# Kernel tuning notes

Measured on AMD Instinct MI355X. Metric: run time of the kernel, lower is better.

## Reference

```python
import jax, jax.numpy as jnp
import numpy as np

EPS = 1e-5  # torch BatchNorm default eps
B, C, T, NOUT, NCLS = 4096, 32, 512, 16, 4


def setup_inputs() -> dict:
    key = jax.random.key(0)
    ks = jax.random.split(key, 12)
    s = lambda k, shape: jax.random.normal(k, shape, jnp.float32) * 0.05
    return {
        "de": jax.random.normal(ks[0], (B, C, T), jnp.float32),
        "adj": jax.random.normal(ks[1], (B, C, C), jnp.float32),  # unused by forward (module recomputes corr)
        "dw_w": s(ks[2], (C, 1, 3)),      # depthwise Conv1d weight [C,1,3]
        "dw_b": s(ks[3], (C,)),
        "pw_w": s(ks[4], (C, C)),          # pointwise 1x1 conv [out,in]
        "pw_b": s(ks[5], (C,)),
        "bn1_g": jnp.ones((C,), jnp.float32),
        "bn1_b": jnp.zeros((C,), jnp.float32),
        "gc_w": s(ks[6], (T, NOUT)),       # GraphConvolution weight
        "fc_w": s(ks[7], (C * NOUT, C)),   # fc62 Linear(512,32)
        "fc_b": s(ks[8], (C,)),
        "bn2_g": jnp.ones((C,), jnp.float32),
        "bn2_b": jnp.zeros((C,), jnp.float32),
        "cls_w": s(ks[9], (C, NCLS)),      # fcclass Linear(32,4)
        "cls_b": s(ks[10], (NCLS,)),
    }


def reference(de, adj, dw_w, dw_b, pw_w, pw_b, bn1_g, bn1_b, gc_w,
              fc_w, fc_b, bn2_g, bn2_b, cls_w, cls_b):
    # --- SeparableConv2d (really 1d): depthwise k=3 -> pointwise 1x1 -> BN -> relu ---
    x = jax.lax.conv_general_dilated(
        de, dw_w, window_strides=(1,), padding=[(1, 1)],
        dimension_numbers=("NCH", "OIH", "NCH"),
        feature_group_count=de.shape[1]) + dw_b[None, :, None]
    x = jnp.einsum("oc,bct->bot", pw_w, x) + pw_b[None, :, None]
    m = x.mean((0, 2), keepdims=True)
    v = x.var((0, 2), keepdims=True)  # biased, as BN normalization uses
    x = (x - m) / jnp.sqrt(v + EPS) * bn1_g[None, :, None] + bn1_b[None, :, None]
    x = jax.nn.relu(x)                       # [B, C, T]

    # --- batched Pearson corrcoef over the time axis (vectorizes the per-sample loop) ---
    xt = x.transpose(0, 2, 1)                # [B, T, C]
    Tn = xt.shape[1]
    f = (Tn - 1) / Tn
    xc = xt - xt.mean(1, keepdims=True)
    num = jnp.einsum("btn,btm->bnm", xc, xc) / Tn   # biased covariance
    var = xt.var(1, ddof=1)                         # torch var default unbiased
    den = jnp.sqrt(var[:, :, None] * var[:, None, :]) * f
    cor = num / den                          # [B, C, C]

    # --- Chebyshev graph convolution (single K term, adj = cor) + relu ---
    g = jnp.einsum("bnm,bmt->bnt", cor, x)   # message passing over channel graph
    g = jax.nn.relu(jnp.einsum("bnt,to->bno", g, gc_w))  # [B, C, 16]

    # --- fc62: Linear -> BN1d -> (dropout: identity) -> sigmoid ---
    h = g.reshape(g.shape[0], -1) @ fc_w + fc_b          # [B, 32]
    m2 = h.mean(0)
    v2 = h.var(0)
    h = (h - m2) / jnp.sqrt(v2 + EPS) * bn2_g + bn2_b
    h = jax.nn.sigmoid(h)

    return h @ cls_w + cls_b                 # [B, 4]
```

## Files before the change

kernel.cpp:

```cpp
#include <hip/hip_runtime.h>
#include <math.h>

#define BB 4096
#define CC 32
#define TT 512
#define NOUTC 16
#define EPSF 1e-5f
#define XS 520


typedef __attribute__((ext_vector_type(16))) float f32x16;
typedef __attribute__((ext_vector_type(4)))  float f32x4;
typedef __attribute__((ext_vector_type(8)))  short short8;
typedef __attribute__((ext_vector_type(8)))  _Float16 half8;
typedef __attribute__((ext_vector_type(4)))  unsigned int u32x4;
typedef __attribute__((ext_vector_type(2)))  unsigned int u32x2;
typedef __attribute__((ext_vector_type(2)))  float vf2;
typedef __attribute__((ext_vector_type(4)))  float vf4;
typedef vf4 __attribute__((aligned(4))) vf4u;
typedef vf2 __attribute__((aligned(4))) vf2u;

__device__ __forceinline__ unsigned short f2b(float f) {
  unsigned int u = __builtin_bit_cast(unsigned int, f);
  return (unsigned short)((u + 0x7FFFu + ((u >> 16) & 1u)) >> 16);
}
__device__ __forceinline__ float blo(unsigned int u) {
  return __builtin_bit_cast(float, u << 16);
}
__device__ __forceinline__ float bhi(unsigned int u) {
  return __builtin_bit_cast(float, u & 0xFFFF0000u);
}
__device__ __forceinline__ unsigned int pk2(float a, float b) {
  return (unsigned int)f2b(a) | ((unsigned int)f2b(b) << 16);
}
__device__ __forceinline__ unsigned short h16(float f) {
  _Float16 h = (_Float16)f;
  return __builtin_bit_cast(unsigned short, h);
}
__device__ __forceinline__ unsigned int h2pk(float a, float b) {
  return (unsigned int)h16(a) | ((unsigned int)h16(b) << 16);
}

__device__ __forceinline__ void conv_cols(const float* __restrict__ deb,
    const float* __restrict__ dw, const float* __restrict__ db_,
    int tid, float* x1A, float* x1B) {
  int t0 = tid * 2;
  int off = (tid == 0) ? 0 : ((tid == 255) ? t0 - 2 : t0 - 1);
#pragma unroll
  for (int c = 0; c < CC; c++) {
    vf4u v = *reinterpret_cast<const vf4u*>(deb + c * TT + off);
    float vm1 = (tid == 0) ? 0.f : ((tid == 255) ? v.y : v.x);
    float v0  = (tid == 0) ? v.x : ((tid == 255) ? v.z : v.y);
    float vp1 = (tid == 0) ? v.y : ((tid == 255) ? v.w : v.z);
    float vp2 = (tid == 0) ? v.z : ((tid == 255) ? 0.f : v.w);
    float w0 = dw[c * 3], w1 = dw[c * 3 + 1], w2 = dw[c * 3 + 2], bc = db_[c];
    x1A[c] = fmaf(w0, vm1, fmaf(w1, v0, fmaf(w2, vp1, bc)));
    x1B[c] = fmaf(w0, v0, fmaf(w1, vp1, fmaf(w2, vp2, bc)));
  }
}

__device__ __forceinline__ void load_af(half8 af[3][2], const float* __restrict__ pw,
                                        const float* __restrict__ dw, int m31, int kh) {
#pragma unroll
  for (int s = 0; s < 2; s++) {
#pragma unroll
    for (int j = 0; j < 8; j++) {
      int c = s * 16 + kh * 8 + j;
      float pv = pw[m31 * CC + c];
#pragma unroll
      for (int k = 0; k < 3; k++) af[k][s][j] = (_Float16)(pv * dw[c * 3 + k]);
    }
  }
}

__global__ __launch_bounds__(256, 3) void k1_stats(const float* __restrict__ de,
    const float* __restrict__ dw, const float* __restrict__ db_,
    const float* __restrict__ pw, const float* __restrict__ pwb,
    float* __restrict__ part, unsigned int* __restrict__ x2h, int useWs) {
  __shared__ __align__(16) unsigned short ldsX[2][258 * 40];
  __shared__ float pbe_s[CC];
  __shared__ float sqb[4][64];

  int tid = threadIdx.x, b = blockIdx.x;
  int lane = tid & 63, w = tid >> 6;
  int m31 = lane & 31, kh = lane >> 5;
  int p2 = tid >> 6, rq = tid & 63;
  int c0 = 8 * p2;

  const float* deb = de + (size_t)b * CC * TT;

  vf4 vq0[8], vq1[8];
#pragma unroll
  for (int cc = 0; cc < 8; cc++) {
    vq0[cc] = *(const vf4u*)(deb + (c0 + cc) * TT + 4 * rq);
    vq1[cc] = *(const vf4u*)(deb + (c0 + cc) * TT + 256 + 4 * rq);
  }
  int ec = tid & 31, es = (tid >> 5) & 1;
  float ev = 0.f;
  if (tid < 64) ev = deb[ec * TT + (es ? 255 : 256)];

  half8 af[3][2];
  load_af(af, pw, dw, m31, kh);
  if (tid < CC) {
    float s = pwb[tid];
#pragma unroll
    for (int c = 0; c < CC; c++) s = fmaf(pw[tid * CC + c], db_[c], s);
    pbe_s[tid] = s;
  }

#pragma unroll
  for (int cc = 0; cc < 8; cc += 2) {
#pragma unroll
    for (int j = 0; j < 4; j++) {
      int r = 4 * rq + 1 + j;
      *(unsigned int*)&ldsX[0][r * 40 + c0 + cc] = h2pk(vq0[cc][j], vq0[cc + 1][j]);
      *(unsigned int*)&ldsX[1][r * 40 + c0 + cc] = h2pk(vq1[cc][j], vq1[cc + 1][j]);
    }
  }
  if (tid < 64) {
    if (es == 0) ldsX[0][257 * 40 + ec] = h16(ev);
    else         ldsX[1][0 * 40 + ec]   = h16(ev);
  } else if (tid < 128) {
    if (es == 0) ldsX[0][0 * 40 + ec] = 0;
    else         ldsX[1][257 * 40 + ec] = 0;
  }
  __syncthreads();

  unsigned int* xw = x2h + (size_t)b * (CC * 256);
  float sA[16], qA[16];
#pragma unroll
  for (int r = 0; r < 16; r++) { sA[r] = 0.f; qA[r] = 0.f; }

#pragma unroll
  for (int h = 0; h < 2; h++) {
    const unsigned short* xf = ldsX[h];
#pragma unroll
    for (int i = 0; i < 2; i++) {
      int wt = w * 2 + i;
      f32x16 acc;
#pragma unroll
      for (int r = 0; r < 16; r++) acc[r] = 0.f;
      int rowb = wt * 32 + m31;
#pragma unroll
      for (int k = 0; k < 3; k++) {
#pragma unroll
        for (int s = 0; s < 2; s++) {
          half8 bf = *(const half8*)&xf[(rowb + k) * 40 + s * 16 + kh * 8];
          acc = __builtin_amdgcn_mfma_f32_32x32x16_f16(af[k][s], bf, acc, 0, 0, 0);
        }
      }
#pragma unroll
      for (int q4 = 0; q4 < 4; q4++) {
        int ob = 8 * q4 + 4 * kh;
        float v0 = acc[4 * q4 + 0] + pbe_s[ob + 0];
        float v1 = acc[4 * q4 + 1] + pbe_s[ob + 1];
        float v2 = acc[4 * q4 + 2] + pbe_s[ob + 2];
        float v3 = acc[4 * q4 + 3] + pbe_s[ob + 3];
        sA[4 * q4 + 0] += v0; qA[4 * q4 + 0] = fmaf(v0, v0, qA[4 * q4 + 0]);
        sA[4 * q4 + 1] += v1; qA[4 * q4 + 1] = fmaf(v1, v1, qA[4 * q4 + 1]);
        sA[4 * q4 + 2] += v2; qA[4 * q4 + 2] = fmaf(v2, v2, qA[4 * q4 + 2]);
        sA[4 * q4 + 3] += v3; qA[4 * q4 + 3] = fmaf(v3, v3, qA[4 * q4 + 3]);
        if (useWs) {
          u32x2 pr2;
          pr2[0] = pk2(v0, v1);
          pr2[1] = pk2(v2, v3);
          *(u32x2*)(xw + ((((size_t)h * 8 + wt) * 4 + q4) * 2 + kh) * 64 + m31 * 2) = pr2;
        }
      }
    }
  }

#pragma unroll
  for (int r = 0; r < 16; r++) {
    float s = sA[r], q = qA[r];
#pragma unroll
    for (int d = 1; d < 32; d <<= 1) { s += __shfl_xor(s, d); q += __shfl_xor(q, d); }
    sA[r] = s; qA[r] = q;
  }
  if (m31 == 0) {
#pragma unroll
    for (int r = 0; r < 16; r++) {
      int o = (r & 3) + 8 * (r >> 2) + 4 * kh;
      sqb[w][o * 2 + 0] = sA[r];
      sqb[w][o * 2 + 1] = qA[r];
    }
  }
  __syncthreads();
  if (tid < 64) {
    int o = tid >> 1, st = tid & 1;
    float v = sqb[0][tid] + sqb[1][tid] + sqb[2][tid] + sqb[3][tid];
    part[(size_t)(st * 32 + o) * BB + b] = v;
  }
}

__global__ void k2_bn1(const float* __restrict__ part, const float* __restrict__ g,
                       const float* __restrict__ bta, float* __restrict__ ws,
                       const float* __restrict__ gcw, unsigned short* __restrict__ gcf) {
  __shared__ float redS[256], redQ[256];
  int o = blockIdx.x, tid = threadIdx.x;
  {
    int i = o * 256 + tid;
    int e = i & 7, ln = (i >> 3) & 63, j = (i >> 9) & 7, w2 = i >> 12;
    int q = ln >> 4, n16 = ln & 15;
    int t = w2 * 256 + q * 8 + j * 32 + e;
    gcf[i] = f2b(gcw[t * 16 + n16]);
  }
  const float* ps = part + (size_t)o * BB;
  const float* pq = part + (size_t)(CC + o) * BB;
  float s = 0, q = 0;
  for (int i = tid; i < BB; i += 256) { s += ps[i]; q += pq[i]; }
  redS[tid] = s; redQ[tid] = q;
  __syncthreads();
  for (int k = 128; k > 0; k >>= 1) {
    if (tid < k) { redS[tid] += redS[tid + k]; redQ[tid] += redQ[tid + k]; }
    __syncthreads();
  }
  if (tid == 0) {
    float N = (float)BB * (float)TT;
    float mean = redS[0] / N;
    float var = redQ[0] / N - mean * mean;
    float sc = g[o] / sqrtf(var + EPSF);
    ws[o] = sc;
    ws[32 + o] = bta[o] - mean * sc;
  }
}

__global__ __launch_bounds__(256, 3) void k3_main(const float* __restrict__ de,
    const float* __restrict__ dw, const float* __restrict__ db_,
    const float* __restrict__ pw, const float* __restrict__ pwb,
    const float* __restrict__ wsv, const unsigned short* __restrict__ gcf,
    const float* __restrict__ fcw, const float* __restrict__ fcb,
    float* __restrict__ hT, const unsigned int* __restrict__ x2h, int useWs) {
  __shared__ __align__(16) unsigned short x_s[CC * XS];
  __shared__ float gramP[2][CC * CC];
  __shared__ float zP[2][CC * NOUTC];
  __shared__ float red16[CC * 8];
  __shared__ float mu_s[CC], inv_s[CC];
  __shared__ float scsh[64];

  int tid = threadIdx.x, b = blockIdx.x;
  int w = tid >> 6, lane = tid & 63;
  int t0 = tid * 2;

  if (tid < 64) scsh[tid] = wsv[tid];
  __syncthreads();

  if (useWs) {
    const unsigned int* xr = x2h + (size_t)b * (CC * 256);
#pragma unroll
    for (int it = 0; it < 16; it++) {
      int g = it * 256 + tid;
      int m31g = g & 31, khg = (g >> 5) & 1, q4g = (g >> 6) & 3;
      int wtg = (g >> 8) & 7, hg = (g >> 11) & 1;
      u32x2 v = *(const u32x2*)(xr + (size_t)g * 2);
      int ob = 8 * q4g + 4 * khg;
      int t = hg * 256 + wtg * 32 + m31g;
      float f0 = fmaxf(fmaf(blo(v[0]), scsh[ob + 0], scsh[32 + ob + 0]), 0.f);
      float f1 = fmaxf(fmaf(bhi(v[0]), scsh[ob + 1], scsh[32 + ob + 1]), 0.f);
      float f2 = fmaxf(fmaf(blo(v[1]), scsh[ob + 2], scsh[32 + ob + 2]), 0.f);
      float f3 = fmaxf(fmaf(bhi(v[1]), scsh[ob + 3], scsh[32 + ob + 3]), 0.f);
      x_s[(ob + 0) * XS + t] = f2b(f0);
      x_s[(ob + 1) * XS + t] = f2b(f1);
      x_s[(ob + 2) * XS + t] = f2b(f2);
      x_s[(ob + 3) * XS + t] = f2b(f3);
    }
  } else {
    const float* deb = de + (size_t)b * CC * TT;
    float x1A[CC], x1B[CC];
    conv_cols(deb, dw, db_, tid, x1A, x1B);
#pragma unroll
    for (int o = 0; o < CC; o++) {
      float aA = pwb[o], aB = pwb[o];
#pragma unroll
      for (int c = 0; c < CC; c++) { float pv = pw[o * CC + c]; aA = fmaf(pv, x1A[c], aA); aB = fmaf(pv, x1B[c], aB); }
      float sc = scsh[o], sh = scsh[32 + o];
      unsigned short hA = f2b(fmaxf(fmaf(aA, sc, sh), 0.f));
      unsigned short hB = f2b(fmaxf(fmaf(aB, sc, sh), 0.f));
      *(unsigned int*)(&x_s[o * XS + t0]) = (unsigned int)hA | ((unsigned int)hB << 16);
    }
  }
  __syncthreads();

  {
    int c = tid >> 3, j = tid & 7;
    float s = 0.f;
#pragma unroll
    for (int it = 0; it < 8; it++) {
      u32x4 u = *reinterpret_cast<const u32x4*>(&x_s[c * XS + j * 64 + it * 8]);
#pragma unroll
      for (int k = 0; k < 4; k++) s += blo(u[k]) + bhi(u[k]);
    }
    red16[c * 8 + j] = s;
  }

  if (w < 2) {
    int m = lane & 31, kh = lane >> 5;
    f32x16 acc;
#pragma unroll
    for (int r = 0; r < 16; r++) acc[r] = 0.f;
    int kbase = w * 256 + kh * 8;
#pragma unroll
    for (int kk = 0; kk < 256; kk += 16) {
      short8 a = *(const short8*)(&x_s[m * XS + kbase + kk]);
      acc = __builtin_amdgcn_mfma_f32_32x32x16_bf16(a, a, acc, 0, 0, 0);
    }
#pragma unroll
    for (int r = 0; r < 16; r++) {
      int row = (r & 3) + 8 * (r >> 2) + 4 * kh;
      gramP[w][row * CC + m] = acc[r];
    }
  } else {
    int w2 = w - 2;
    int n16 = lane & 15, q = lane >> 4;
    f32x4 ac0, ac1;
#pragma unroll
    for (int r = 0; r < 4; r++) { ac0[r] = 0.f; ac1[r] = 0.f; }
    const unsigned short* gf = gcf + w2 * 4096;
    short8 bfr[8];
#pragma unroll
    for (int j = 0; j < 8; j++) bfr[j] = *(const short8*)(gf + (j * 64 + lane) * 8);
    int kbase = w2 * 256 + q * 8;
#pragma unroll
    for (int j = 0; j < 8; j++) {
      int kk = j * 32;
      short8 af0 = *(const short8*)(&x_s[n16 * XS + kbase + kk]);
      short8 af1 = *(const short8*)(&x_s[(16 + n16) * XS + kbase + kk]);
      ac0 = __builtin_amdgcn_mfma_f32_16x16x32_bf16(af0, bfr[j], ac0, 0, 0, 0);
      ac1 = __builtin_amdgcn_mfma_f32_16x16x32_bf16(af1, bfr[j], ac1, 0, 0, 0);
    }
#pragma unroll
    for (int r = 0; r < 4; r++) {
      int row = q * 4 + r;
      zP[w2][row * NOUTC + n16] = ac0[r];
      zP[w2][(16 + row) * NOUTC + n16] = ac1[r];
    }
  }
  __syncthreads();
  if (tid < CC) {
    float s = 0.f;
#pragma unroll
    for (int j = 0; j < 8; j++) s += red16[tid * 8 + j];
    mu_s[tid] = s;
  }
  __syncthreads();
  float* gram0 = gramP[0];
  float* Zi = zP[0];
  float* g2 = zP[1];
  for (int i = tid; i < CC * CC; i += 256) {
    int n = i >> 5, m = i & 31;
    gram0[i] = gram0[i] + gramP[1][i] - mu_s[n] * mu_s[m] * (1.f / (float)TT);
  }
  for (int i = tid; i < CC * NOUTC; i += 256) Zi[i] = zP[0][i] + zP[1][i];
  __syncthreads();
  if (tid < CC) inv_s[tid] = rsqrtf(gram0[tid * 32 + tid]);
  __syncthreads();
  for (int i = tid; i < CC * NOUTC; i += 256) {
    int n = i >> 4, o = i & 15;
    float s = 0.f;
#pragma unroll
    for (int m = 0; m < CC; m++) s = fmaf(gram0[n * 32 + m] * inv_s[m], Zi[m * NOUTC + o], s);
    g2[i] = fmaxf(s * inv_s[n], 0.f);
  }
  __syncthreads();
  float* red2 = gramP[1];
  {
    int j = tid & 31, ch = tid >> 5;
    float pacc = 0.f;
#pragma unroll
    for (int ii = 0; ii < 64; ii++) {
      int i = ch * 64 + ii;
      pacc = fmaf(g2[i], fcw[i * CC + j], pacc);
    }
    red2[j * 9 + ch] = pacc;
  }
  __syncthreads();
  if (tid < CC) {
    float h = fcb[tid];
#pragma unroll
    for (int ch = 0; ch < 8; ch++) h += red2[tid * 9 + ch];
    hT[(size_t)tid * BB + b] = h;
  }
}

__global__ void k4_bn2(const float* __restrict__ hT, const float* __restrict__ g,
                       const float* __restrict__ bta, float* __restrict__ ws) {
  __shared__ float redS[256], redQ[256];
  int j = blockIdx.x, tid = threadIdx.x;
  const float* row = hT + (size_t)j * BB;
  float s = 0, q = 0;
  for (int i = tid; i < BB; i += 256) { float v = row[i]; s += v; q = fmaf(v, v, q); }
  redS[tid] = s; redQ[tid] = q;
  __syncthreads();
  for (int k = 128; k > 0; k >>= 1) {
    if (tid < k) { redS[tid] += redS[tid + k]; redQ[tid] += redQ[tid + k]; }
    __syncthreads();
  }
  if (tid == 0) {
    float N = (float)BB;
    float mean = redS[0] / N;
    float var = redQ[0] / N - mean * mean;
    float sc = g[j] / sqrtf(var + EPSF);
    ws[64 + j] = sc;
    ws[96 + j] = bta[j] - mean * sc;
  }
}

__global__ void k5_out(const float* __restrict__ hT, const float* __restrict__ ws,
                       const float* __restrict__ clsw, const float* __restrict__ clsb,
                       float* __restrict__ out) {
  __shared__ float hs[CC * 257];
  int b0 = blockIdx.x * 256, tid = threadIdx.x;
  for (int i = tid; i < CC * 256; i += 256) {
    int j = i >> 8, bb = i & 255;
    float v = fmaf(hT[(size_t)j * BB + b0 + bb], ws[64 + j], ws[96 + j]);
    hs[j * 257 + bb] = 1.f / (1.f + expf(-v));
  }
  __syncthreads();
  float o0 = clsb[0], o1 = clsb[1], o2 = clsb[2], o3 = clsb[3];
#pragma unroll
  for (int j = 0; j < CC; j++) {
    float h = hs[j * 257 + tid];
    o0 = fmaf(h, clsw[j * 4 + 0], o0);
    o1 = fmaf(h, clsw[j * 4 + 1], o1);
    o2 = fmaf(h, clsw[j * 4 + 2], o2);
    o3 = fmaf(h, clsw[j * 4 + 3], o3);
  }
  float4* out4 = reinterpret_cast<float4*>(out);
  out4[b0 + tid] = make_float4(o0, o1, o2, o3);
}

extern "C" void kernel_launch(void* const* d_in, const int* in_sizes, int n_in,
                              void* d_out, int out_size, void* d_ws, size_t ws_size,
                              hipStream_t stream) {
  const float* de   = (const float*)d_in[0];
  const float* dw   = (const float*)d_in[2];
  const float* db_  = (const float*)d_in[3];
  const float* pw   = (const float*)d_in[4];
  const float* pwb  = (const float*)d_in[5];
  const float* bn1g = (const float*)d_in[6];
  const float* bn1b = (const float*)d_in[7];
  const float* gcw  = (const float*)d_in[8];
  const float* fcw  = (const float*)d_in[9];
  const float* fcb  = (const float*)d_in[10];
  const float* bn2g = (const float*)d_in[11];
  const float* bn2b = (const float*)d_in[12];
  const float* clsw = (const float*)d_in[13];
  const float* clsb = (const float*)d_in[14];

  float* ws = (float*)d_ws;
  unsigned short* gcf = (unsigned short*)(ws + 128);
  float* hT   = ws + 4224;
  float* part = ws + 135296;
  unsigned int* x2h = (unsigned int*)(ws + 397440);
  float* out  = (float*)d_out;

  size_t need = ((size_t)397440 + 33554432ull) * 4ull;
  int useWs = (ws_size >= need) ? 1 : 0;

  k1_stats<<<BB, 256, 0, stream>>>(de, dw, db_, pw, pwb, part, x2h, useWs);
  k2_bn1<<<CC, 256, 0, stream>>>(part, bn1g, bn1b, ws, gcw, gcf);
  k3_main<<<BB, 256, 0, stream>>>(de, dw, db_, pw, pwb, ws, gcf, fcw, fcb, hT, x2h, useWs);
  k4_bn2<<<CC, 256, 0, stream>>>(hT, bn2g, bn2b, ws);
  k5_out<<<BB / 256, 256, 0, stream>>>(hT, ws, clsw, clsb, out);
}
```

Baseline: 477.7 us.

## Process two samples per block in k1 with register-prefetched half-tiles

The stats kernel now runs 2048 blocks, each handling two batch samples. While the MFMA work runs on one LDS half-buffer, the block prefetches the next half or next sample from global memory into registers, hiding load latency behind compute. Per-wave partial sums are written straight to global memory, which drops the shared-memory reduction; the partial array grows fourfold and k2 sums the extra entries. In exchange the kernel has more syncthreads, higher register pressure and a larger workspace requirement.

```diff
diff --git a/kernel.cpp b/kernel.cpp
--- a/kernel.cpp
+++ b/kernel.cpp
@@ -79,25 +79,12 @@
     float* __restrict__ part, unsigned int* __restrict__ x2h, int useWs) {
   __shared__ __align__(16) unsigned short ldsX[2][258 * 40];
   __shared__ float pbe_s[CC];
-  __shared__ float sqb[4][64];
-
-  int tid = threadIdx.x, b = blockIdx.x;
+
+  int tid = threadIdx.x, blk = blockIdx.x;
   int lane = tid & 63, w = tid >> 6;
   int m31 = lane & 31, kh = lane >> 5;
-  int p2 = tid >> 6, rq = tid & 63;
-  int c0 = 8 * p2;
-
-  const float* deb = de + (size_t)b * CC * TT;
-
-  vf4 vq0[8], vq1[8];
-#pragma unroll
-  for (int cc = 0; cc < 8; cc++) {
-    vq0[cc] = *(const vf4u*)(deb + (c0 + cc) * TT + 4 * rq);
-    vq1[cc] = *(const vf4u*)(deb + (c0 + cc) * TT + 256 + 4 * rq);
-  }
-  int ec = tid & 31, es = (tid >> 5) & 1;
-  float ev = 0.f;
-  if (tid < 64) ev = deb[ec * TT + (es ? 255 : 256)];
+  int rq = tid & 63;
+  int c0 = 8 * w;
 
   half8 af[3][2];
   load_af(af, pw, dw, m31, kh);
@@ -107,33 +94,29 @@
     for (int c = 0; c < CC; c++) s = fmaf(pw[tid * CC + c], db_[c], s);
     pbe_s[tid] = s;
   }
-
-#pragma unroll
-  for (int cc = 0; cc < 8; cc += 2) {
-#pragma unroll
-    for (int j = 0; j < 4; j++) {
-      int r = 4 * rq + 1 + j;
-      *(unsigned int*)&ldsX[0][r * 40 + c0 + cc] = h2pk(vq0[cc][j], vq0[cc + 1][j]);
-      *(unsigned int*)&ldsX[1][r * 40 + c0 + cc] = h2pk(vq1[cc][j], vq1[cc + 1][j]);
-    }
-  }
-  if (tid < 64) {
-    if (es == 0) ldsX[0][257 * 40 + ec] = h16(ev);
-    else         ldsX[1][0 * 40 + ec]   = h16(ev);
-  } else if (tid < 128) {
-    if (es == 0) ldsX[0][0 * 40 + ec] = 0;
-    else         ldsX[1][257 * 40 + ec] = 0;
-  }
-  __syncthreads();
-
-  unsigned int* xw = x2h + (size_t)b * (CC * 256);
+  if (tid < 32) { ldsX[0][tid] = 0; ldsX[1][257 * 40 + tid] = 0; }
+
+  vf4 R0[8], R1[8];
+  {
+    const float* de0 = de + (size_t)blk * CC * TT;
+#pragma unroll
+    for (int cc = 0; cc < 8; cc++) {
+      R0[cc] = *(const vf4u*)(de0 + (c0 + cc) * TT + 4 * rq);
+      R1[cc] = *(const vf4u*)(de0 + (c0 + cc) * TT + 256 + 4 * rq);
+    }
+#pragma unroll
+    for (int cc = 0; cc < 8; cc += 2) {
+#pragma unroll
+      for (int j = 0; j < 4; j++)
+        *(unsigned int*)&ldsX[0][(4 * rq + 1 + j) * 40 + c0 + cc] = h2pk(R0[cc][j], R0[cc + 1][j]);
+    }
+  }
+
   float sA[16], qA[16];
 #pragma unroll
   for (int r = 0; r < 16; r++) { sA[r] = 0.f; qA[r] = 0.f; }
 
-#pragma unroll
-  for (int h = 0; h < 2; h++) {
-    const unsigned short* xf = ldsX[h];
+  auto COMPUTE = [&](const unsigned short* xf, int h, unsigned int* xw) {
 #pragma unroll
     for (int i = 0; i < 2; i++) {
       int wt = w * 2 + i;
@@ -168,28 +151,66 @@
         }
       }
     }
-  }
-
-#pragma unroll
-  for (int r = 0; r < 16; r++) {
-    float s = sA[r], q = qA[r];
-#pragma unroll
-    for (int d = 1; d < 32; d <<= 1) { s += __shfl_xor(s, d); q += __shfl_xor(q, d); }
-    sA[r] = s; qA[r] = q;
-  }
-  if (m31 == 0) {
+  };
+
+  for (int s = 0; s < 2; ++s) {
+    size_t b_s = (size_t)blk + (size_t)s * 2048;
+    unsigned int* xw = x2h + b_s * (CC * 256);
+
+    __syncthreads();
+#pragma unroll
+    for (int cc = 0; cc < 8; cc += 2) {
+#pragma unroll
+      for (int j = 0; j < 4; j++)
+        *(unsigned int*)&ldsX[1][(4 * rq + 1 + j) * 40 + c0 + cc] = h2pk(R1[cc][j], R1[cc + 1][j]);
+    }
+    if (rq == 63) {
+#pragma unroll
+      for (int cc = 0; cc < 8; cc += 2)
+        *(unsigned int*)&ldsX[1][c0 + cc] = h2pk(R0[cc][3], R0[cc + 1][3]);
+    }
+    if (rq == 0) {
+#pragma unroll
+      for (int cc = 0; cc < 8; cc += 2)
+        *(unsigned int*)&ldsX[0][257 * 40 + c0 + cc] = h2pk(R1[cc][0], R1[cc + 1][0]);
+    }
+    if (s < 1) {
+      const float* den = de + ((size_t)blk + 2048) * CC * TT;
+#pragma unroll
+      for (int cc = 0; cc < 8; cc++)
+        R0[cc] = *(const vf4u*)(den + (c0 + cc) * TT + 4 * rq);
+    }
+    __syncthreads();
+    COMPUTE(ldsX[0], 0, xw);
+
+    __syncthreads();
+    if (s < 1) {
+#pragma unroll
+      for (int cc = 0; cc < 8; cc += 2) {
+#pragma unroll
+        for (int j = 0; j < 4; j++)
+          *(unsigned int*)&ldsX[0][(4 * rq + 1 + j) * 40 + c0 + cc] = h2pk(R0[cc][j], R0[cc + 1][j]);
+      }
+      const float* den = de + ((size_t)blk + 2048) * CC * TT;
+#pragma unroll
+      for (int cc = 0; cc < 8; cc++)
+        R1[cc] = *(const vf4u*)(den + (c0 + cc) * TT + 256 + 4 * rq);
+    }
+    __syncthreads();
+    COMPUTE(ldsX[1], 1, xw);
+
 #pragma unroll
     for (int r = 0; r < 16; r++) {
-      int o = (r & 3) + 8 * (r >> 2) + 4 * kh;
-      sqb[w][o * 2 + 0] = sA[r];
-      sqb[w][o * 2 + 1] = qA[r];
-    }
-  }
-  __syncthreads();
-  if (tid < 64) {
-    int o = tid >> 1, st = tid & 1;
-    float v = sqb[0][tid] + sqb[1][tid] + sqb[2][tid] + sqb[3][tid];
-    part[(size_t)(st * 32 + o) * BB + b] = v;
+      float ss = sA[r], qq = qA[r];
+#pragma unroll
+      for (int d = 1; d < 32; d <<= 1) { ss += __shfl_xor(ss, d); qq += __shfl_xor(qq, d); }
+      if (m31 == 0) {
+        int o = (r & 3) + 8 * (r >> 2) + 4 * kh;
+        part[((size_t)o * 4 + w) * BB + b_s] = ss;
+        part[(((size_t)(32 + o)) * 4 + w) * BB + b_s] = qq;
+      }
+      sA[r] = 0.f; qA[r] = 0.f;
+    }
   }
 }
 
@@ -205,10 +226,10 @@
     int t = w2 * 256 + q * 8 + j * 32 + e;
     gcf[i] = f2b(gcw[t * 16 + n16]);
   }
-  const float* ps = part + (size_t)o * BB;
-  const float* pq = part + (size_t)(CC + o) * BB;
+  const float* ps = part + (size_t)o * 4 * BB;
+  const float* pq = part + (size_t)(CC + o) * 4 * BB;
   float s = 0, q = 0;
-  for (int i = tid; i < BB; i += 256) { s += ps[i]; q += pq[i]; }
+  for (int i = tid; i < 4 * BB; i += 256) { s += ps[i]; q += pq[i]; }
   redS[tid] = s; redQ[tid] = q;
   __syncthreads();
   for (int k = 128; k > 0; k >>= 1) {
@@ -451,13 +472,13 @@
   unsigned short* gcf = (unsigned short*)(ws + 128);
   float* hT   = ws + 4224;
   float* part = ws + 135296;
-  unsigned int* x2h = (unsigned int*)(ws + 397440);
+  unsigned int* x2h = (unsigned int*)(ws + 1183872);
   float* out  = (float*)d_out;
 
-  size_t need = ((size_t)397440 + 33554432ull) * 4ull;
+  size_t need = ((size_t)1183872 + 33554432ull) * 4ull;
   int useWs = (ws_size >= need) ? 1 : 0;
 
-  k1_stats<<<BB, 256, 0, stream>>>(de, dw, db_, pw, pwb, part, x2h, useWs);
+  k1_stats<<<2048, 256, 0, stream>>>(de, dw, db_, pw, pwb, part, x2h, useWs);
   k2_bn1<<<CC, 256, 0, stream>>>(part, bn1g, bn1b, ws, gcw, gcf);
   k3_main<<<BB, 256, 0, stream>>>(de, dw, db_, pw, pwb, ws, gcf, fcw, fcb, hT, x2h, useWs);
   k4_bn2<<<CC, 256, 0, stream>>>(hT, bn2g, bn2b, ws);
```

Result: slower. 647.5 us (+35.5%).
